# Performance work log

Measured on AMD Instinct MI355X. Metric: run time of the kernel, lower is better.

Reference implementation:

```python
import jax, jax.numpy as jnp
import numpy as np

EMBED_DIM = 768
NUM_HEADS = 12
HEAD_DIM = EMBED_DIM // NUM_HEADS


def setup_inputs() -> dict:
    key = jax.random.key(0)
    ks = jax.random.split(key, 12)
    B, T, D, Hp, Wp = 4, 32, EMBED_DIM, 16, 16
    h = jax.random.normal(ks[0], (B, T, D, Hp, Wp), dtype=jnp.float32)
    u_enc = jax.random.uniform(ks[1], (B, T, D, Hp, Wp), dtype=jnp.float32)
    lam = jax.random.uniform(ks[2], (B, T, 1, Hp, Wp), dtype=jnp.float32)
    s = 1.0 / np.sqrt(D)
    Wq = jax.random.normal(ks[3], (D, D), dtype=jnp.float32) * s
    bq = jnp.zeros((D,), dtype=jnp.float32)
    Wk = jax.random.normal(ks[4], (D, D), dtype=jnp.float32) * s
    bk = jnp.zeros((D,), dtype=jnp.float32)
    Wv = jax.random.normal(ks[5], (D, D), dtype=jnp.float32) * s
    bv = jnp.zeros((D,), dtype=jnp.float32)
    Wo = jax.random.normal(ks[6], (D, D), dtype=jnp.float32) * s
    bo = jnp.zeros((D,), dtype=jnp.float32)
    return {"h": h, "u_enc": u_enc, "lam": lam,
            "Wq": Wq, "bq": bq, "Wk": Wk, "bk": bk,
            "Wv": Wv, "bv": bv, "Wo": Wo, "bo": bo}


def reference(h, u_enc, lam, Wq, bq, Wk, bk, Wv, bv, Wo, bo):
    B, T, D, Hp, Wp = h.shape
    S = Hp * Wp
    NH, HD = NUM_HEADS, HEAD_DIM
    # (B,T,D,Hp,Wp) -> (B*S, T, D)
    h_seq = jnp.transpose(h, (0, 3, 4, 1, 2)).reshape(B * S, T, D)
    u_seq = jnp.transpose(u_enc, (0, 3, 4, 1, 2)).reshape(B * S, T, D)
    lam_seq = jnp.transpose(lam, (0, 3, 4, 1, 2)).reshape(B * S, T)
    # projections (nn.Linear: x @ W.T + b)
    Q = (h_seq @ Wq.T + bq).reshape(B * S, T, NH, HD).transpose(0, 2, 1, 3)
    K = (h_seq @ Wk.T + bk).reshape(B * S, T, NH, HD).transpose(0, 2, 1, 3)
    V = (h_seq @ Wv.T + bv).reshape(B * S, T, NH, HD).transpose(0, 2, 1, 3)
    scores = jnp.einsum('bhqd,bhkd->bhqk', Q, K) / jnp.sqrt(jnp.float32(HD))
    # key-dependent uncertainty penalty: lam_j * mean_d(u_j)
    u_pen = lam_seq * u_seq.mean(axis=-1)  # (B*S, T)
    scores = scores - u_pen[:, None, None, :]
    attn = jax.nn.softmax(scores, axis=-1)  # dropout: eval mode (identity)
    out = jnp.einsum('bhqk,bhkd->bhqd', attn, V)
    out = out.transpose(0, 2, 1, 3).reshape(B * S, T, D)
    out = out @ Wo.T + bo
    return jnp.transpose(out.reshape(B, Hp, Wp, T, D), (0, 3, 4, 1, 2))
```

## Files before the change

### kernel.cpp

```cpp
#include <hip/hip_runtime.h>

typedef float   f32x4 __attribute__((ext_vector_type(4)));
typedef _Float16 f16x8 __attribute__((ext_vector_type(8)));

#define DEV static __device__ __forceinline__

#define BB 4
#define TT 32
#define DD 768
#define SS 256
#define NHD 12
#define HD 64
#define NSEQ  (BB*SS)
#define MTOK  (NSEQ*TT)

DEV void async_copy16(const _Float16* g, _Float16* l) {
  __builtin_amdgcn_global_load_lds(
      (const __attribute__((address_space(1))) unsigned int*)g,
      (__attribute__((address_space(3))) unsigned int*)l,
      16, 0, 0);
}

DEV int swz_chunk(int r, int kc) {
  return r * 4 + (kc ^ (r & 3) ^ ((r >> 2) & 3));
}

__global__ __launch_bounds__(256) void k_transpose_h(const float* __restrict__ h,
                                                     _Float16* __restrict__ A) {
  __shared__ _Float16 Tl[256 * 65];
  const int slab = blockIdx.x;
  const int d0   = blockIdx.y * 64;
  const int t    = threadIdx.x;
  const float4* hv = (const float4*)(h + (slab * DD + d0) * SS);
  #pragma unroll
  for (int i = 0; i < 16; ++i) {
    int dd = i * 4 + (t >> 6);
    int s4 = (t & 63) * 4;
    float4 v = hv[dd * 64 + (t & 63)];
    Tl[(s4 + 0) * 65 + dd] = (_Float16)v.x;
    Tl[(s4 + 1) * 65 + dd] = (_Float16)v.y;
    Tl[(s4 + 2) * 65 + dd] = (_Float16)v.z;
    Tl[(s4 + 3) * 65 + dd] = (_Float16)v.w;
  }
  __syncthreads();
  #pragma unroll
  for (int p = 0; p < 8; ++p) {
    int s  = p * 32 + (t >> 3);
    int dd = (t & 7) * 8;
    f16x8 val;
    #pragma unroll
    for (int j = 0; j < 8; ++j) val[j] = Tl[s * 65 + dd + j];
    *(f16x8*)(A + (slab * SS + s) * DD + d0 + dd) = val;
  }
}

__global__ __launch_bounds__(256) void k_convert_w(const float* __restrict__ Wq,
                                                   const float* __restrict__ Wk,
                                                   const float* __restrict__ Wv,
                                                   const float* __restrict__ Wo,
                                                   _Float16* __restrict__ WQKV,
                                                   _Float16* __restrict__ WoH) {
  int idx = blockIdx.x * 256 + threadIdx.x;
  int row = idx / 96;
  int c8  = (idx % 96) * 8;
  const float* src; _Float16* dst;
  if (row < 768)       { src = Wq + row * 768;          dst = WQKV + row * 768; }
  else if (row < 1536) { src = Wk + (row - 768) * 768;  dst = WQKV + row * 768; }
  else if (row < 2304) { src = Wv + (row - 1536) * 768; dst = WQKV + row * 768; }
  else                 { src = Wo + (row - 2304) * 768; dst = WoH  + (row - 2304) * 768; }
  float4 v0 = *(const float4*)(src + c8);
  float4 v1 = *(const float4*)(src + c8 + 4);
  f16x8 o;
  o[0]=(_Float16)v0.x; o[1]=(_Float16)v0.y; o[2]=(_Float16)v0.z; o[3]=(_Float16)v0.w;
  o[4]=(_Float16)v1.x; o[5]=(_Float16)v1.y; o[6]=(_Float16)v1.z; o[7]=(_Float16)v1.w;
  *(f16x8*)(dst + c8) = o;
}

__global__ __launch_bounds__(256) void k_upen(const float* __restrict__ u,
                                              const float* __restrict__ lam,
                                              float* __restrict__ upen) {
  int slab = blockIdx.x >> 2;
  int q    = blockIdx.x & 3;
  int s    = threadIdx.x;
  const float* base = u + (slab * DD + q * 192) * SS + s;
  float sum = 0.f;
  for (int d = 0; d < 192; ++d) sum += base[d * SS];
  int b = slab >> 5, tt = slab & 31;
  float l = lam[slab * SS + s];
  atomicAdd(&upen[(b * SS + s) * TT + tt], sum * l * (1.0f / 768.0f));
}

__global__ __launch_bounds__(256, 2) void k_gemm_qkv(const _Float16* __restrict__ A,
                                                     const _Float16* __restrict__ Bw,
                                                     const float* __restrict__ bq,
                                                     const float* __restrict__ bk,
                                                     const float* __restrict__ bv,
                                                     _Float16* __restrict__ Qp,
                                                     _Float16* __restrict__ Kp,
                                                     _Float16* __restrict__ Vp) {
  __shared__ _Float16 As[128 * 32];
  __shared__ _Float16 Bs[256 * 32];
  const int mt = blockIdx.x & 255, nt = blockIdx.x >> 8;
  const int m0 = mt * 128, n0 = nt * 256;
  const int tid = threadIdx.x, w = tid >> 6, lane = tid & 63;
  const int wr = (w >> 1) * 64, wcc = (w & 1) * 128;
  f32x4 acc[4][8] = {};
  for (int it = 0; it < 24; ++it) {
    const int k0 = it * 32;
    __syncthreads();
    #pragma unroll
    for (int i = 0; i < 2; ++i) {
      int c = tid + 256 * i;
      int row = c >> 2;
      int coff = ((c & 3) ^ (row & 3) ^ ((row >> 2) & 3)) * 8;
      _Float16* ldsA = (_Float16*)((char*)As + (w * 1024 + i * 4096 + lane * 16));
      async_copy16(A + (m0 + row) * DD + k0 + coff, ldsA);
    }
    #pragma unroll
    for (int i = 0; i < 4; ++i) {
      int c = tid + 256 * i;
      int row = c >> 2;
      int coff = ((c & 3) ^ (row & 3) ^ ((row >> 2) & 3)) * 8;
      _Float16* ldsB = (_Float16*)((char*)Bs + (w * 1024 + i * 4096 + lane * 16));
      async_copy16(Bw + (n0 + row) * DD + k0 + coff, ldsB);
    }
    __syncthreads();
    f16x8 af[4], bf[8];
    #pragma unroll
    for (int mi = 0; mi < 4; ++mi)
      af[mi] = *(const f16x8*)&As[swz_chunk(wr + mi * 16 + (lane & 15), lane >> 4) * 8];
    #pragma unroll
    for (int ni = 0; ni < 8; ++ni)
      bf[ni] = *(const f16x8*)&Bs[swz_chunk(wcc + ni * 16 + (lane & 15), lane >> 4) * 8];
    #pragma unroll
    for (int mi = 0; mi < 4; ++mi)
      #pragma unroll
      for (int ni = 0; ni < 8; ++ni)
        acc[mi][ni] = __builtin_amdgcn_mfma_f32_16x16x32_f16(af[mi], bf[ni], acc[mi][ni], 0, 0, 0);
  }
  const int sel = nt / 3;
  const float scale = (sel == 0) ? 0.125f : 1.0f;
  const float* bias = (sel == 0) ? bq : ((sel == 1) ? bk : bv);
  _Float16* dst = (sel == 0) ? Qp : ((sel == 1) ? Kp : Vp);
  const int slab = mt >> 1, s0 = (mt & 1) * 128;
  const int b = slab >> 5, t = slab & 31;
  #pragma unroll
  for (int ni = 0; ni < 8; ++ni) {
    int n768 = nt * 256 - sel * 768 + wcc + ni * 16 + (lane & 15);
    int head = n768 >> 6, hd = n768 & 63;
    float bs = bias[n768];
    long hb = (long)head * 2048 + t * 64 + hd;
    #pragma unroll
    for (int mi = 0; mi < 4; ++mi) {
      f32x4 v = acc[mi][ni];
      #pragma unroll
      for (int r = 0; r < 4; ++r) {
        int s = s0 + wr + mi * 16 + (lane >> 4) * 4 + r;
        long seq = b * 256 + s;
        dst[seq * 24576 + hb] = (_Float16)((v[r] + bs) * scale);
      }
    }
  }
}

__global__ __launch_bounds__(256) void k_attn(const _Float16* __restrict__ Qp,
                                              const _Float16* __restrict__ Kp,
                                              const _Float16* __restrict__ Vp,
                                              const float* __restrict__ upen,
                                              _Float16* __restrict__ O) {
  __shared__ _Float16 lds[4][32 * 66 + 32 * 40];
  const int w = threadIdx.x >> 6, lane = threadIdx.x & 63;
  const int seq = blockIdx.x / 3, hg = blockIdx.x % 3;
  const int head = hg * 4 + w;
  const int b = seq >> 8, s = seq & 255;
  _Float16* Vs = &lds[w][0];
  _Float16* Ps = &lds[w][32 * 66];
  const long base = (long)(seq * NHD + head) * 2048;
  const _Float16* Qb = Qp + base;
  const _Float16* Kb = Kp + base;
  const _Float16* Vb = Vp + base;

  {
    int t = lane & 31, hh = (lane >> 5) * 32;
    f16x8 vc[4];
    #pragma unroll
    for (int c = 0; c < 4; ++c) vc[c] = *(const f16x8*)(Vb + t * 64 + hh + c * 8);
    #pragma unroll
    for (int c = 0; c < 4; ++c)
      #pragma unroll
      for (int p = 0; p < 4; ++p) {
        union { _Float16 h[2]; unsigned u; } pk;
        pk.h[0] = vc[c][2 * p]; pk.h[1] = vc[c][2 * p + 1];
        *(unsigned*)&Vs[t * 66 + hh + c * 8 + 2 * p] = pk.u;
      }
  }
  f16x8 qf[2][2], kf[2][2];
  #pragma unroll
  for (int i = 0; i < 2; ++i)
    #pragma unroll
    for (int ks = 0; ks < 2; ++ks) {
      int off = (i * 16 + (lane & 15)) * 64 + ks * 32 + (lane >> 4) * 8;
      qf[i][ks] = *(const f16x8*)(Qb + off);
      kf[i][ks] = *(const f16x8*)(Kb + off);
    }
  f32x4 sc[2][2] = {};
  #pragma unroll
  for (int mq = 0; mq < 2; ++mq)
    #pragma unroll
    for (int nk = 0; nk < 2; ++nk)
      #pragma unroll
      for (int ks = 0; ks < 2; ++ks)
        sc[mq][nk] = __builtin_amdgcn_mfma_f32_16x16x32_f16(qf[mq][ks], kf[nk][ks], sc[mq][nk], 0, 0, 0);

  const float up0 = upen[seq * TT + (lane & 15)];
  const float up1 = upen[seq * TT + 16 + (lane & 15)];

  #pragma unroll
  for (int mq = 0; mq < 2; ++mq) {
    #pragma unroll
    for (int r = 0; r < 4; ++r) {
      float s0 = sc[mq][0][r] - up0;
      float s1 = sc[mq][1][r] - up1;
      float mx = fmaxf(s0, s1);
      #pragma unroll
      for (int off = 1; off < 16; off <<= 1) mx = fmaxf(mx, __shfl_xor(mx, off, 64));
      float e0 = __expf(s0 - mx), e1 = __expf(s1 - mx);
      float sum = e0 + e1;
      #pragma unroll
      for (int off = 1; off < 16; off <<= 1) sum += __shfl_xor(sum, off, 64);
      float inv = 1.0f / sum;
      int row = mq * 16 + (lane >> 4) * 4 + r;
      Ps[row * 40 + (lane & 15)]      = (_Float16)(e0 * inv);
      Ps[row * 40 + 16 + (lane & 15)] = (_Float16)(e1 * inv);
    }
  }
  f16x8 pf[2];
  #pragma unroll
  for (int mq = 0; mq < 2; ++mq)
    pf[mq] = *(const f16x8*)(Ps + (mq * 16 + (lane & 15)) * 40 + (lane >> 4) * 8);
  f32x4 oacc[2][4] = {};
  #pragma unroll
  for (int nh = 0; nh < 4; ++nh) {
    int hd = nh * 16 + (lane & 15);
    f16x8 vf;
    #pragma unroll
    for (int j = 0; j < 8; ++j) vf[j] = Vs[((lane >> 4) * 8 + j) * 66 + hd];
    #pragma unroll
    for (int mq = 0; mq < 2; ++mq)
      oacc[mq][nh] = __builtin_amdgcn_mfma_f32_16x16x32_f16(pf[mq], vf, oacc[mq][nh], 0, 0, 0);
  }
  #pragma unroll
  for (int mq = 0; mq < 2; ++mq)
    #pragma unroll
    for (int nh = 0; nh < 4; ++nh) {
      int hd = nh * 16 + (lane & 15);
      #pragma unroll
      for (int r = 0; r < 4; ++r) {
        int t = mq * 16 + (lane >> 4) * 4 + r;
        O[((long)((b << 5) + t) * SS + s) * DD + head * HD + hd] = (_Float16)oacc[mq][nh][r];
      }
    }
}

__global__ __launch_bounds__(256, 2) void k_gemm_out(const _Float16* __restrict__ Wn,
                                                     const _Float16* __restrict__ O,
                                                     const float* __restrict__ bo,
                                                     float* __restrict__ out) {
  __shared__ _Float16 As[128 * 32];
  __shared__ _Float16 Bs[256 * 32];
  const int ct = blockIdx.x & 127, rt = blockIdx.x >> 7;
  const int R0 = rt * 128, C0 = ct * 256;
  const int tid = threadIdx.x, w = tid >> 6, lane = tid & 63;
  const int wr = (w >> 1) * 64, wcc = (w & 1) * 128;
  f32x4 acc[4][8] = {};
  for (int it = 0; it < 24; ++it) {
    const int k0 = it * 32;
    __syncthreads();
    #pragma unroll
    for (int i = 0; i < 2; ++i) {
      int c = tid + 256 * i;
      int row = c >> 2;
      int coff = ((c & 3) ^ (row & 3) ^ ((row >> 2) & 3)) * 8;
      _Float16* ldsA = (_Float16*)((char*)As + (w * 1024 + i * 4096 + lane * 16));
      async_copy16(Wn + (R0 + row) * DD + k0 + coff, ldsA);
    }
    #pragma unroll
    for (int i = 0; i < 4; ++i) {
      int c = tid + 256 * i;
      int row = c >> 2;
      int coff = ((c & 3) ^ (row & 3) ^ ((row >> 2) & 3)) * 8;
      _Float16* ldsB = (_Float16*)((char*)Bs + (w * 1024 + i * 4096 + lane * 16));
      async_copy16(O + (C0 + row) * DD + k0 + coff, ldsB);
    }
    __syncthreads();
    f16x8 af[4], bf[8];
    #pragma unroll
    for (int ri = 0; ri < 4; ++ri)
      af[ri] = *(const f16x8*)&As[swz_chunk(wr + ri * 16 + (lane & 15), lane >> 4) * 8];
    #pragma unroll
    for (int ci = 0; ci < 8; ++ci)
      bf[ci] = *(const f16x8*)&Bs[swz_chunk(wcc + ci * 16 + (lane & 15), lane >> 4) * 8];
    #pragma unroll
    for (int ri = 0; ri < 4; ++ri)
      #pragma unroll
      for (int ci = 0; ci < 8; ++ci)
        acc[ri][ci] = __builtin_amdgcn_mfma_f32_16x16x32_f16(af[ri], bf[ci], acc[ri][ci], 0, 0, 0);
  }
  const int slab = ct;
  #pragma unroll
  for (int ri = 0; ri < 4; ++ri) {
    #pragma unroll
    for (int ci = 0; ci < 8; ++ci) {
      int s = wcc + ci * 16 + (lane & 15);
      f32x4 v = acc[ri][ci];
      #pragma unroll
      for (int r = 0; r < 4; ++r) {
        int R = R0 + wr + ri * 16 + (lane >> 4) * 4 + r;
        out[((long)slab * DD + R) * SS + s] = v[r] + bo[R];
      }
    }
  }
}

extern "C" void kernel_launch(void* const* d_in, const int* in_sizes, int n_in,
                              void* d_out, int out_size, void* d_ws, size_t ws_size,
                              hipStream_t stream) {
  const float* h   = (const float*)d_in[0];
  const float* u   = (const float*)d_in[1];
  const float* lam = (const float*)d_in[2];
  const float* Wq  = (const float*)d_in[3];
  const float* bq  = (const float*)d_in[4];
  const float* Wk  = (const float*)d_in[5];
  const float* bk  = (const float*)d_in[6];
  const float* Wv  = (const float*)d_in[7];
  const float* bv  = (const float*)d_in[8];
  const float* Wo  = (const float*)d_in[9];
  const float* bo  = (const float*)d_in[10];
  float* out = (float*)d_out;

  char* ws = (char*)d_ws;
  _Float16* Abuf = (_Float16*)(ws);
  _Float16* WQKV = (_Float16*)(ws + 50331648);
  _Float16* WoH  = (_Float16*)(ws + 53870592);
  float*    upen = (float*)   (ws + 55050240);
  _Float16* Qp   = (_Float16*)(ws + 55181312);
  _Float16* Kp   = (_Float16*)(ws + 105512960);
  _Float16* Vp   = (_Float16*)(ws + 155844608);

  hipMemsetAsync(upen, 0, 32768 * sizeof(float), stream);
  k_transpose_h<<<dim3(128, 12), 256, 0, stream>>>(h, Abuf);
  k_convert_w<<<1152, 256, 0, stream>>>(Wq, Wk, Wv, Wo, WQKV, WoH);
  k_upen<<<512, 256, 0, stream>>>(u, lam, upen);
  k_gemm_qkv<<<256 * 9, 256, 0, stream>>>(Abuf, WQKV, bq, bk, bv, Qp, Kp, Vp);
  k_attn<<<1024 * 3, 256, 0, stream>>>(Qp, Kp, Vp, upen, Abuf);
  k_gemm_out<<<128 * 6, 256, 0, stream>>>(WoH, Abuf, bo, out);
}
```

Baseline: 533.3 us.

## Double-buffer LDS tiles in QKV and output projection GEMMs

Both projection GEMMs now keep two LDS buffers and issue the async global-to-LDS copies for the next K-slice before computing on the current one. A single barrier per iteration replaces the two it had before. The goal is to hide global load latency behind the MFMA work. LDS use doubles to 48KB per block, which may limit the two-blocks-per-CU occupancy, and correctness relies on the async LDS loads being complete at the barrier.

```diff
diff --git a/kernel.cpp b/kernel.cpp
--- a/kernel.cpp
+++ b/kernel.cpp
@@ -98,45 +98,53 @@
                                                      _Float16* __restrict__ Qp,
                                                      _Float16* __restrict__ Kp,
                                                      _Float16* __restrict__ Vp) {
-  __shared__ _Float16 As[128 * 32];
-  __shared__ _Float16 Bs[256 * 32];
+  __shared__ _Float16 As[2][128 * 32];
+  __shared__ _Float16 Bs[2][256 * 32];
   const int mt = blockIdx.x & 255, nt = blockIdx.x >> 8;
   const int m0 = mt * 128, n0 = nt * 256;
   const int tid = threadIdx.x, w = tid >> 6, lane = tid & 63;
   const int wr = (w >> 1) * 64, wcc = (w & 1) * 128;
   f32x4 acc[4][8] = {};
-  for (int it = 0; it < 24; ++it) {
-    const int k0 = it * 32;
-    __syncthreads();
+
+  auto stage = [&](int buf, int k0) {
     #pragma unroll
     for (int i = 0; i < 2; ++i) {
       int c = tid + 256 * i;
       int row = c >> 2;
       int coff = ((c & 3) ^ (row & 3) ^ ((row >> 2) & 3)) * 8;
-      _Float16* ldsA = (_Float16*)((char*)As + (w * 1024 + i * 4096 + lane * 16));
-      async_copy16(A + (m0 + row) * DD + k0 + coff, ldsA);
+      async_copy16(A + (m0 + row) * DD + k0 + coff,
+                   (_Float16*)((char*)&As[buf][0] + tid * 16 + i * 4096));
     }
     #pragma unroll
     for (int i = 0; i < 4; ++i) {
       int c = tid + 256 * i;
       int row = c >> 2;
       int coff = ((c & 3) ^ (row & 3) ^ ((row >> 2) & 3)) * 8;
-      _Float16* ldsB = (_Float16*)((char*)Bs + (w * 1024 + i * 4096 + lane * 16));
-      async_copy16(Bw + (n0 + row) * DD + k0 + coff, ldsB);
-    }
-    __syncthreads();
+      async_copy16(Bw + (n0 + row) * DD + k0 + coff,
+                   (_Float16*)((char*)&Bs[buf][0] + tid * 16 + i * 4096));
+    }
+  };
+
+  stage(0, 0);
+  __syncthreads();
+  for (int it = 0; it < 24; ++it) {
+    const int cur = it & 1;
+    if (it < 23) stage(cur ^ 1, (it + 1) * 32);
+    const _Float16* Ac = &As[cur][0];
+    const _Float16* Bc = &Bs[cur][0];
     f16x8 af[4], bf[8];
     #pragma unroll
     for (int mi = 0; mi < 4; ++mi)
-      af[mi] = *(const f16x8*)&As[swz_chunk(wr + mi * 16 + (lane & 15), lane >> 4) * 8];
+      af[mi] = *(const f16x8*)&Ac[swz_chunk(wr + mi * 16 + (lane & 15), lane >> 4) * 8];
     #pragma unroll
     for (int ni = 0; ni < 8; ++ni)
-      bf[ni] = *(const f16x8*)&Bs[swz_chunk(wcc + ni * 16 + (lane & 15), lane >> 4) * 8];
+      bf[ni] = *(const f16x8*)&Bc[swz_chunk(wcc + ni * 16 + (lane & 15), lane >> 4) * 8];
     #pragma unroll
     for (int mi = 0; mi < 4; ++mi)
       #pragma unroll
       for (int ni = 0; ni < 8; ++ni)
         acc[mi][ni] = __builtin_amdgcn_mfma_f32_16x16x32_f16(af[mi], bf[ni], acc[mi][ni], 0, 0, 0);
+    __syncthreads();
   }
   const int sel = nt / 3;
   const float scale = (sel == 0) ? 0.125f : 1.0f;
@@ -266,45 +274,53 @@
                                                      const _Float16* __restrict__ O,
                                                      const float* __restrict__ bo,
                                                      float* __restrict__ out) {
-  __shared__ _Float16 As[128 * 32];
-  __shared__ _Float16 Bs[256 * 32];
+  __shared__ _Float16 As[2][128 * 32];
+  __shared__ _Float16 Bs[2][256 * 32];
   const int ct = blockIdx.x & 127, rt = blockIdx.x >> 7;
   const int R0 = rt * 128, C0 = ct * 256;
   const int tid = threadIdx.x, w = tid >> 6, lane = tid & 63;
   const int wr = (w >> 1) * 64, wcc = (w & 1) * 128;
   f32x4 acc[4][8] = {};
-  for (int it = 0; it < 24; ++it) {
-    const int k0 = it * 32;
-    __syncthreads();
+
+  auto stage = [&](int buf, int k0) {
     #pragma unroll
     for (int i = 0; i < 2; ++i) {
       int c = tid + 256 * i;
       int row = c >> 2;
       int coff = ((c & 3) ^ (row & 3) ^ ((row >> 2) & 3)) * 8;
-      _Float16* ldsA = (_Float16*)((char*)As + (w * 1024 + i * 4096 + lane * 16));
-      async_copy16(Wn + (R0 + row) * DD + k0 + coff, ldsA);
+      async_copy16(Wn + (R0 + row) * DD + k0 + coff,
+                   (_Float16*)((char*)&As[buf][0] + tid * 16 + i * 4096));
     }
     #pragma unroll
     for (int i = 0; i < 4; ++i) {
       int c = tid + 256 * i;
       int row = c >> 2;
       int coff = ((c & 3) ^ (row & 3) ^ ((row >> 2) & 3)) * 8;
-      _Float16* ldsB = (_Float16*)((char*)Bs + (w * 1024 + i * 4096 + lane * 16));
-      async_copy16(O + (C0 + row) * DD + k0 + coff, ldsB);
-    }
-    __syncthreads();
+      async_copy16(O + (C0 + row) * DD + k0 + coff,
+                   (_Float16*)((char*)&Bs[buf][0] + tid * 16 + i * 4096));
+    }
+  };
+
+  stage(0, 0);
+  __syncthreads();
+  for (int it = 0; it < 24; ++it) {
+    const int cur = it & 1;
+    if (it < 23) stage(cur ^ 1, (it + 1) * 32);
+    const _Float16* Ac = &As[cur][0];
+    const _Float16* Bc = &Bs[cur][0];
     f16x8 af[4], bf[8];
     #pragma unroll
     for (int ri = 0; ri < 4; ++ri)
-      af[ri] = *(const f16x8*)&As[swz_chunk(wr + ri * 16 + (lane & 15), lane >> 4) * 8];
+      af[ri] = *(const f16x8*)&Ac[swz_chunk(wr + ri * 16 + (lane & 15), lane >> 4) * 8];
     #pragma unroll
     for (int ci = 0; ci < 8; ++ci)
-      bf[ci] = *(const f16x8*)&Bs[swz_chunk(wcc + ci * 16 + (lane & 15), lane >> 4) * 8];
+      bf[ci] = *(const f16x8*)&Bc[swz_chunk(wcc + ci * 16 + (lane & 15), lane >> 4) * 8];
     #pragma unroll
     for (int ri = 0; ri < 4; ++ri)
       #pragma unroll
       for (int ci = 0; ci < 8; ++ci)
         acc[ri][ci] = __builtin_amdgcn_mfma_f32_16x16x32_f16(af[ri], bf[ci], acc[ri][ci], 0, 0, 0);
+    __syncthreads();
   }
   const int slab = ct;
   #pragma unroll
```

Result: no change. 543.1 us (+1.8%).

## Restructure QKV GEMM with 256x256 tiles, double-buffered LDS and block swizzle

Applied to the files above, without the earlier changes.

Rewrites the QKV projection GEMM to use 512-thread blocks computing 256x256 tiles with a K-step of 64. The two LDS buffers let the next tile's async global-to-LDS loads overlap the current tile's MFMA work, and fragment loads are interleaved with compute under setprio hints. A block-index swizzle groups tiles for L2 reuse. This cuts loop iterations and sync overhead but needs 128KB of LDS per block and more accumulators per thread, which may limit occupancy.

```diff
diff --git a/kernel.cpp b/kernel.cpp
--- a/kernel.cpp
+++ b/kernel.cpp
@@ -90,7 +90,7 @@
   atomicAdd(&upen[(b * SS + s) * TT + tt], sum * l * (1.0f / 768.0f));
 }
 
-__global__ __launch_bounds__(256, 2) void k_gemm_qkv(const _Float16* __restrict__ A,
+__global__ __launch_bounds__(512, 2) void k_gemm_qkv(const _Float16* __restrict__ A,
                                                      const _Float16* __restrict__ Bw,
                                                      const float* __restrict__ bq,
                                                      const float* __restrict__ bk,
@@ -98,65 +98,97 @@
                                                      _Float16* __restrict__ Qp,
                                                      _Float16* __restrict__ Kp,
                                                      _Float16* __restrict__ Vp) {
-  __shared__ _Float16 As[128 * 32];
-  __shared__ _Float16 Bs[256 * 32];
-  const int mt = blockIdx.x & 255, nt = blockIdx.x >> 8;
-  const int m0 = mt * 128, n0 = nt * 256;
-  const int tid = threadIdx.x, w = tid >> 6, lane = tid & 63;
-  const int wr = (w >> 1) * 64, wcc = (w & 1) * 128;
-  f32x4 acc[4][8] = {};
-  for (int it = 0; it < 24; ++it) {
-    const int k0 = it * 32;
-    __syncthreads();
-    #pragma unroll
-    for (int i = 0; i < 2; ++i) {
-      int c = tid + 256 * i;
-      int row = c >> 2;
-      int coff = ((c & 3) ^ (row & 3) ^ ((row >> 2) & 3)) * 8;
-      _Float16* ldsA = (_Float16*)((char*)As + (w * 1024 + i * 4096 + lane * 16));
-      async_copy16(A + (m0 + row) * DD + k0 + coff, ldsA);
-    }
-    #pragma unroll
-    for (int i = 0; i < 4; ++i) {
-      int c = tid + 256 * i;
-      int row = c >> 2;
-      int coff = ((c & 3) ^ (row & 3) ^ ((row >> 2) & 3)) * 8;
-      _Float16* ldsB = (_Float16*)((char*)Bs + (w * 1024 + i * 4096 + lane * 16));
-      async_copy16(Bw + (n0 + row) * DD + k0 + coff, ldsB);
-    }
-    __syncthreads();
-    f16x8 af[4], bf[8];
-    #pragma unroll
-    for (int mi = 0; mi < 4; ++mi)
-      af[mi] = *(const f16x8*)&As[swz_chunk(wr + mi * 16 + (lane & 15), lane >> 4) * 8];
-    #pragma unroll
-    for (int ni = 0; ni < 8; ++ni)
-      bf[ni] = *(const f16x8*)&Bs[swz_chunk(wcc + ni * 16 + (lane & 15), lane >> 4) * 8];
-    #pragma unroll
-    for (int mi = 0; mi < 4; ++mi)
-      #pragma unroll
-      for (int ni = 0; ni < 8; ++ni)
-        acc[mi][ni] = __builtin_amdgcn_mfma_f32_16x16x32_f16(af[mi], bf[ni], acc[mi][ni], 0, 0, 0);
-  }
+  __shared__ __align__(16) _Float16 As[2][256 * 64];
+  __shared__ __align__(16) _Float16 Bs[2][256 * 64];
+  const int swz = (blockIdx.x & 7) * 144 + (blockIdx.x >> 3);
+  const int mt = swz / 9, nt = swz - mt * 9;
+  const int m0 = mt * 256, n0 = nt * 256;
+  const int tid = threadIdx.x, lane = tid & 63, w = tid >> 6;
+  const int wm = w >> 2, wn = w & 3;
+  f32x4 acc[8][4] = {};
+
+  auto stage = [&](const _Float16* __restrict__ g, int grow0, _Float16* l, int k0) {
+    #pragma unroll
+    for (int li = 0; li < 4; ++li) {
+      int cc = tid + 512 * li;
+      int row = cc >> 3;
+      int kc = (cc & 7) ^ (row & 7);
+      async_copy16(g + (grow0 + row) * DD + k0 + kc * 8, l + cc * 8);
+    }
+  };
+
+  stage(A, m0, &As[0][0], 0);
+  stage(Bw, n0, &Bs[0][0], 0);
+  __syncthreads();
+
+  for (int it = 0; it < 12; ++it) {
+    const int cb = it & 1;
+    const _Float16* Ac = &As[cb][0];
+    const _Float16* Bc = &Bs[cb][0];
+    const int kn = (it + 1) * 64;
+    f16x8 bfr[4][2];
+    #pragma unroll
+    for (int p = 0; p < 4; ++p) {
+      f16x8 afr[2][2];
+      #pragma unroll
+      for (int q = 0; q < 2; ++q)
+        #pragma unroll
+        for (int kk = 0; kk < 2; ++kk) {
+          int row = wm * 128 + (2 * p + q) * 16 + (lane & 15);
+          int kc = kk * 4 + (lane >> 4);
+          afr[q][kk] = *(const f16x8*)&Ac[row * 64 + (kc ^ (row & 7)) * 8];
+        }
+      if (p == 0) {
+        #pragma unroll
+        for (int ni = 0; ni < 4; ++ni)
+          #pragma unroll
+          for (int kk = 0; kk < 2; ++kk) {
+            int row = wn * 64 + ni * 16 + (lane & 15);
+            int kc = kk * 4 + (lane >> 4);
+            bfr[ni][kk] = *(const f16x8*)&Bc[row * 64 + (kc ^ (row & 7)) * 8];
+          }
+        if (it < 11) stage(A, m0, &As[cb ^ 1][0], kn);
+      }
+      if (p == 1 && it < 11) stage(Bw, n0, &Bs[cb ^ 1][0], kn);
+      __builtin_amdgcn_s_barrier();
+      asm volatile("s_waitcnt lgkmcnt(0)" ::: "memory");
+      __builtin_amdgcn_sched_barrier(0);
+      __builtin_amdgcn_s_setprio(1);
+      #pragma unroll
+      for (int q = 0; q < 2; ++q)
+        #pragma unroll
+        for (int ni = 0; ni < 4; ++ni) {
+          acc[2 * p + q][ni] = __builtin_amdgcn_mfma_f32_16x16x32_f16(
+              afr[q][0], bfr[ni][0], acc[2 * p + q][ni], 0, 0, 0);
+          acc[2 * p + q][ni] = __builtin_amdgcn_mfma_f32_16x16x32_f16(
+              afr[q][1], bfr[ni][1], acc[2 * p + q][ni], 0, 0, 0);
+        }
+      __builtin_amdgcn_s_setprio(0);
+      __builtin_amdgcn_s_barrier();
+    }
+    asm volatile("s_waitcnt vmcnt(0)" ::: "memory");
+    __builtin_amdgcn_sched_barrier(0);
+    __builtin_amdgcn_s_barrier();
+  }
+
   const int sel = nt / 3;
   const float scale = (sel == 0) ? 0.125f : 1.0f;
   const float* bias = (sel == 0) ? bq : ((sel == 1) ? bk : bv);
   _Float16* dst = (sel == 0) ? Qp : ((sel == 1) ? Kp : Vp);
-  const int slab = mt >> 1, s0 = (mt & 1) * 128;
-  const int b = slab >> 5, t = slab & 31;
-  #pragma unroll
-  for (int ni = 0; ni < 8; ++ni) {
-    int n768 = nt * 256 - sel * 768 + wcc + ni * 16 + (lane & 15);
+  const int b = mt >> 5, t = mt & 31;
+  #pragma unroll
+  for (int ni = 0; ni < 4; ++ni) {
+    int n768 = nt * 256 - sel * 768 + wn * 64 + ni * 16 + (lane & 15);
     int head = n768 >> 6, hd = n768 & 63;
     float bs = bias[n768];
     long hb = (long)head * 2048 + t * 64 + hd;
     #pragma unroll
-    for (int mi = 0; mi < 4; ++mi) {
+    for (int mi = 0; mi < 8; ++mi) {
       f32x4 v = acc[mi][ni];
       #pragma unroll
       for (int r = 0; r < 4; ++r) {
-        int s = s0 + wr + mi * 16 + (lane >> 4) * 4 + r;
-        long seq = b * 256 + s;
+        int s = wm * 128 + mi * 16 + (lane >> 4) * 4 + r;
+        long seq = (long)b * 256 + s;
         dst[seq * 24576 + hb] = (_Float16)((v[r] + bs) * scale);
       }
     }
@@ -351,7 +383,7 @@
   k_transpose_h<<<dim3(128, 12), 256, 0, stream>>>(h, Abuf);
   k_convert_w<<<1152, 256, 0, stream>>>(Wq, Wk, Wv, Wo, WQKV, WoH);
   k_upen<<<512, 256, 0, stream>>>(u, lam, upen);
-  k_gemm_qkv<<<256 * 9, 256, 0, stream>>>(Abuf, WQKV, bq, bk, bv, Qp, Kp, Vp);
+  k_gemm_qkv<<<1152, 512, 0, stream>>>(Abuf, WQKV, bq, bk, bv, Qp, Kp, Vp);
   k_attn<<<1024 * 3, 256, 0, stream>>>(Qp, Kp, Vp, upen, Abuf);
   k_gemm_out<<<128 * 6, 256, 0, stream>>>(WoH, Abuf, bo, out);
 }
```

Result: no change. 532.8 us (-0.1%).
